# Kernel optimization log

Hardware: AMD Instinct MI355X
Metric: run time of the kernel (lower is better)

Reference implementation:

```python
import jax, jax.numpy as jnp
import numpy as np

N, OBS, H, M, L = 512, 32, 128, 128, 3


def _w(key, shape, fan_in):
    return jax.random.normal(key, shape, dtype=jnp.float32) / np.sqrt(fan_in)


def setup_inputs() -> dict:
    key = jax.random.key(0)
    ks = iter(jax.random.split(key, 64))
    inp = {}
    inp["obs"] = jax.random.normal(next(ks), (N, OBS), dtype=jnp.float32)
    inp["pos"] = jax.random.uniform(next(ks), (N, 2), dtype=jnp.float32)
    # encoder: obs_dim -> H -> H -> H
    inp["enc_W1"] = _w(next(ks), (H, OBS), OBS); inp["enc_b1"] = jnp.zeros((H,), jnp.float32)
    inp["enc_W2"] = _w(next(ks), (H, H), H);     inp["enc_b2"] = jnp.zeros((H,), jnp.float32)
    inp["enc_W3"] = _w(next(ks), (H, H), H);     inp["enc_b3"] = jnp.zeros((H,), jnp.float32)
    # per-layer message MLPs: (2H+1) -> M -> M -> M, stacked over L layers
    inp["msg_W1"] = _w(next(ks), (L, M, 2 * H + 1), 2 * H + 1); inp["msg_b1"] = jnp.zeros((L, M), jnp.float32)
    inp["msg_W2"] = _w(next(ks), (L, M, M), M);                 inp["msg_b2"] = jnp.zeros((L, M), jnp.float32)
    inp["msg_W3"] = _w(next(ks), (L, M, M), M);                 inp["msg_b3"] = jnp.zeros((L, M), jnp.float32)
    # per-layer update MLPs: (H+M) -> H -> H -> H, stacked over L layers
    inp["upd_W1"] = _w(next(ks), (L, H, H + M), H + M); inp["upd_b1"] = jnp.zeros((L, H), jnp.float32)
    inp["upd_W2"] = _w(next(ks), (L, H, H), H);         inp["upd_b2"] = jnp.zeros((L, H), jnp.float32)
    inp["upd_W3"] = _w(next(ks), (L, H, H), H);         inp["upd_b3"] = jnp.zeros((L, H), jnp.float32)
    return inp


def _mlp3(x, W1, b1, W2, b2, W3, b3):
    h = jax.nn.relu(x @ W1.T + b1)
    h = jax.nn.relu(h @ W2.T + b2)
    return h @ W3.T + b3


def reference(obs, pos, enc_W1, enc_b1, enc_W2, enc_b2, enc_W3, enc_b3,
              msg_W1, msg_b1, msg_W2, msg_b2, msg_W3, msg_b3,
              upd_W1, upd_b1, upd_W2, upd_b2, upd_W3, upd_b3):
    n = obs.shape[0]
    h = enc_W1.shape[0]
    z = _mlp3(obs, enc_W1, enc_b1, enc_W2, enc_b2, enc_W3, enc_b3)  # (N, H)
    # pairwise distances; guard diagonal sqrt(0) for grad safety, then zero it
    diff = pos[:, None, :] - pos[None, :, :]                  # (N, N, 2)
    sq = jnp.sum(diff * diff, axis=-1)                        # (N, N)
    eye = jnp.eye(n, dtype=pos.dtype)
    dist = jnp.sqrt(jnp.where(eye > 0, 1.0, sq)) * (1.0 - eye)
    nondiag = (1.0 - eye)[:, :, None]
    n_layers = msg_W1.shape[0]
    for l in range(n_layers):
        W1 = msg_W1[l]
        Wi, Wj, wd = W1[:, :h], W1[:, h:2 * h], W1[:, 2 * h]  # split concat [z_i, z_j, d]
        A = z @ Wi.T                                          # (N, M) receiver term
        B = z @ Wj.T                                          # (N, M) sender term
        h1 = jax.nn.relu(A[:, None, :] + B[None, :, :] + dist[:, :, None] * wd + msg_b1[l])  # (N, N, M)
        h2 = jax.nn.relu(jnp.einsum('ijm,km->ijk', h1, msg_W2[l]) + msg_b2[l])
        m = jnp.einsum('ijm,km->ijk', h2, msg_W3[l]) + msg_b3[l]
        m = m * nondiag                                       # exclude j == i
        msum = jnp.sum(m, axis=1)                             # (N, M) sum over senders j
        z = _mlp3(jnp.concatenate([z, msum], axis=-1),
                  upd_W1[l], upd_b1[l], upd_W2[l], upd_b2[l], upd_W3[l], upd_b3[l])
    return z
```

## Files before the change

### kernel.cpp

```cpp
#include <hip/hip_runtime.h>

#define NA 512
#define NOBS 32
#define NH 128

typedef const float* fp32p;
typedef __attribute__((ext_vector_type(8))) short bf16x8;
typedef __attribute__((ext_vector_type(4))) float f32x4;

__device__ __forceinline__ short f2bf(float f) {
    union { float f; unsigned u; } v; v.f = f;
    unsigned r = v.u + 0x7fffu + ((v.u >> 16) & 1u);
    return (short)(r >> 16);
}

__device__ __forceinline__ bf16x8 wfrag_f4(const float* p) {
    float4 u = *(const float4*)p;
    float4 v = *(const float4*)(p + 4);
    bf16x8 f;
    f[0] = f2bf(u.x); f[1] = f2bf(u.y); f[2] = f2bf(u.z); f[3] = f2bf(u.w);
    f[4] = f2bf(v.x); f[5] = f2bf(v.y); f[6] = f2bf(v.z); f[7] = f2bf(v.w);
    return f;
}

#define HSTR 136

__global__ __launch_bounds__(128) void encoder_kernel(
    fp32p obs, fp32p W1, fp32p b1, fp32p W2, fp32p b2, fp32p W3, fp32p b3,
    float* __restrict__ z) {
    __shared__ float xs[NOBS];
    __shared__ float h1s[NH];
    __shared__ float h2s[NH];
    const int i = blockIdx.x, t = threadIdx.x;
    if (t < NOBS) xs[t] = obs[i * NOBS + t];
    __syncthreads();
    float a = b1[t];
    for (int k = 0; k < NOBS; ++k) a += xs[k] * W1[t * NOBS + k];
    h1s[t] = fmaxf(a, 0.0f);
    __syncthreads();
    a = b2[t];
    for (int k = 0; k < NH; ++k) a += h1s[k] * W2[t * NH + k];
    h2s[t] = fmaxf(a, 0.0f);
    __syncthreads();
    a = b3[t];
    for (int k = 0; k < NH; ++k) a += h2s[k] * W3[t * NH + k];
    z[i * NH + t] = a;
}

__global__ __launch_bounds__(128) void ab_kernel(
    const float* __restrict__ z, fp32p W1l, float* __restrict__ A, float* __restrict__ B) {
    __shared__ float zs[NH];
    const int i = blockIdx.x, m = threadIdx.x;
    zs[m] = z[i * NH + m];
    __syncthreads();
    const float* wr = W1l + m * 257;
    float a = 0.0f, b = 0.0f;
    for (int k = 0; k < NH; ++k) {
        float zk = zs[k];
        a += zk * wr[k];
        b += zk * wr[NH + k];
    }
    A[i * NH + m] = a;
    B[i * NH + m] = b;
}

__global__ __launch_bounds__(512) void msg_upd_kernel(
    const float* __restrict__ A, const float* __restrict__ B,
    fp32p pos, const float* __restrict__ zin,
    fp32p W1l, fp32p b1, fp32p W2, fp32p b2, fp32p W3, fp32p b3,
    fp32p uW1, fp32p ub1, fp32p uW2, fp32p ub2, fp32p uW3, fp32p ub3,
    fp32p msgW1n, int do_ab,
    float* __restrict__ zout, float* __restrict__ An, float* __restrict__ Bn) {
    const int i = blockIdx.x;
    const int t = threadIdx.x;
    const int lane = t & 63;
    const int w = t >> 6;
    const int q = lane >> 4;
    const int c = lane & 15;
    const int ncol = w * 16 + c;

    __shared__ short h1s[64 * HSTR];
    __shared__ short h2s[64 * HSTR];
    __shared__ float distrow[NA];
    __shared__ float amrow[NH];
    __shared__ float wdsr[NH];
    __shared__ float xs2[2 * NH];
    __shared__ float part[4 * NH];
    __shared__ float part2[4 * NH];
    __shared__ float hx[NH], hy[NH], hz[NH];

    if (t < NH) {
        amrow[t] = A[i * NH + t] + b1[t];
        wdsr[t]  = W1l[t * 257 + 256];
        xs2[t] = zin[(size_t)i * NH + t];
    }
    {
        const float2 pi = *(const float2*)&pos[2 * i];
        const float2 pj = *(const float2*)&pos[2 * t];
        const float dx = pi.x - pj.x, dy = pi.y - pj.y;
        const float s = dx * dx + dy * dy;
        distrow[t] = (t == i) ? 0.0f : sqrtf(s);
    }

    bf16x8 w2f[4], w3f[4];
    {
        const float* w2r = W2 + (size_t)ncol * NH + q * 8;
        const float* w3r = W3 + (size_t)ncol * NH + q * 8;
        #pragma unroll
        for (int kb = 0; kb < 4; ++kb) {
            w2f[kb] = wfrag_f4(w2r + kb * 32);
            w3f[kb] = wfrag_f4(w3r + kb * 32);
        }
    }
    const float b2n = b2[ncol];
    const float b3n = b3[ncol];

    const int m2 = lane * 2;
    float psum = 0.0f;

    for (int c8 = 0; c8 < 8; ++c8) {
        const int j0 = c8 * 64;
        __syncthreads();

        {
            const float am0 = amrow[m2],     am1 = amrow[m2 + 1];
            const float wd0 = wdsr[m2],      wd1 = wdsr[m2 + 1];
            #pragma unroll
            for (int rr = 0; rr < 8; ++rr) {
                const int row = rr * 8 + w;
                const int jg  = j0 + row;
                const float2 bv = *(const float2*)&B[(size_t)jg * NH + m2];
                const float d = distrow[jg];
                const float v0 = fmaxf(am0 + bv.x + d * wd0, 0.0f);
                const float v1 = fmaxf(am1 + bv.y + d * wd1, 0.0f);
                const unsigned p = (unsigned)(unsigned short)f2bf(v0) |
                                   ((unsigned)(unsigned short)f2bf(v1) << 16);
                *(unsigned*)&h1s[row * HSTR + m2] = p;
            }
        }
        __syncthreads();

        #pragma unroll
        for (int jt = 0; jt < 4; ++jt) {
            f32x4 acc = {0.f, 0.f, 0.f, 0.f};
            const short* arow = &h1s[(jt * 16 + c) * HSTR + q * 8];
            #pragma unroll
            for (int kb = 0; kb < 4; ++kb) {
                bf16x8 a = *(const bf16x8*)(arow + kb * 32);
                acc = __builtin_amdgcn_mfma_f32_16x16x32_bf16(a, w2f[kb], acc, 0, 0, 0);
            }
            #pragma unroll
            for (int r = 0; r < 4; ++r) {
                const int row = jt * 16 + q * 4 + r;
                h2s[row * HSTR + ncol] = f2bf(fmaxf(acc[r] + b2n, 0.0f));
            }
        }
        __syncthreads();

        #pragma unroll
        for (int jt = 0; jt < 4; ++jt) {
            f32x4 acc = {0.f, 0.f, 0.f, 0.f};
            const short* arow = &h2s[(jt * 16 + c) * HSTR + q * 8];
            #pragma unroll
            for (int kb = 0; kb < 4; ++kb) {
                bf16x8 a = *(const bf16x8*)(arow + kb * 32);
                acc = __builtin_amdgcn_mfma_f32_16x16x32_bf16(a, w3f[kb], acc, 0, 0, 0);
            }
            #pragma unroll
            for (int r = 0; r < 4; ++r) {
                const int jg = j0 + jt * 16 + q * 4 + r;
                if (jg != i) psum += acc[r] + b3n;
            }
        }
    }

    psum += __shfl_xor(psum, 16, 64);
    psum += __shfl_xor(psum, 32, 64);
    if (lane < 16) xs2[NH + ncol] = psum;
    __syncthreads();

    const int nn = t >> 2;
    const int ks = t & 3;
    {
        const float* wr = uW1 + (size_t)nn * 256 + ks * 4;
        float p = 0.f;
        #pragma unroll
        for (int it = 0; it < 16; ++it) {
            const float4 wv = *(const float4*)(wr + it * 16);
            const float4 xv = *(const float4*)&xs2[it * 16 + ks * 4];
            p += wv.x * xv.x + wv.y * xv.y + wv.z * xv.z + wv.w * xv.w;
        }
        part[ks * NH + nn] = p;
    }
    __syncthreads();
    if (t < NH)
        hx[t] = fmaxf(ub1[t] + part[t] + part[NH + t] + part[2 * NH + t] + part[3 * NH + t], 0.f);
    __syncthreads();
    {
        const float* wr = uW2 + (size_t)nn * NH + ks * 4;
        float p = 0.f;
        #pragma unroll
        for (int it = 0; it < 8; ++it) {
            const float4 wv = *(const float4*)(wr + it * 16);
            const float4 xv = *(const float4*)&hx[it * 16 + ks * 4];
            p += wv.x * xv.x + wv.y * xv.y + wv.z * xv.z + wv.w * xv.w;
        }
        part[ks * NH + nn] = p;
    }
    __syncthreads();
    if (t < NH)
        hy[t] = fmaxf(ub2[t] + part[t] + part[NH + t] + part[2 * NH + t] + part[3 * NH + t], 0.f);
    __syncthreads();
    {
        const float* wr = uW3 + (size_t)nn * NH + ks * 4;
        float p = 0.f;
        #pragma unroll
        for (int it = 0; it < 8; ++it) {
            const float4 wv = *(const float4*)(wr + it * 16);
            const float4 xv = *(const float4*)&hy[it * 16 + ks * 4];
            p += wv.x * xv.x + wv.y * xv.y + wv.z * xv.z + wv.w * xv.w;
        }
        part[ks * NH + nn] = p;
    }
    __syncthreads();
    if (t < NH) {
        const float v = ub3[t] + part[t] + part[NH + t] + part[2 * NH + t] + part[3 * NH + t];
        zout[(size_t)i * NH + t] = v;
        hz[t] = v;
    }
    if (!do_ab) return;
    __syncthreads();
    {
        const float* pr = msgW1n + (size_t)nn * 257;
        float pa = 0.f, pb = 0.f;
        #pragma unroll
        for (int it = 0; it < 8; ++it) {
            #pragma unroll
            for (int j = 0; j < 4; ++j) {
                const int k = it * 16 + ks * 4 + j;
                const float x = hz[k];
                pa += x * pr[k];
                pb += x * pr[NH + k];
            }
        }
        part[ks * NH + nn] = pa;
        part2[ks * NH + nn] = pb;
    }
    __syncthreads();
    if (t < NH) {
        An[(size_t)i * NH + t] = part[t] + part[NH + t] + part[2 * NH + t] + part[3 * NH + t];
        Bn[(size_t)i * NH + t] = part2[t] + part2[NH + t] + part2[2 * NH + t] + part2[3 * NH + t];
    }
}

extern "C" void kernel_launch(void* const* d_in, const int* in_sizes, int n_in,
                              void* d_out, int out_size, void* d_ws, size_t ws_size,
                              hipStream_t stream) {
    fp32p obs   = (fp32p)d_in[0];
    fp32p pos   = (fp32p)d_in[1];
    fp32p encW1 = (fp32p)d_in[2];  fp32p encb1 = (fp32p)d_in[3];
    fp32p encW2 = (fp32p)d_in[4];  fp32p encb2 = (fp32p)d_in[5];
    fp32p encW3 = (fp32p)d_in[6];  fp32p encb3 = (fp32p)d_in[7];
    fp32p msgW1 = (fp32p)d_in[8];  fp32p msgb1 = (fp32p)d_in[9];
    fp32p msgW2 = (fp32p)d_in[10]; fp32p msgb2 = (fp32p)d_in[11];
    fp32p msgW3 = (fp32p)d_in[12]; fp32p msgb3 = (fp32p)d_in[13];
    fp32p updW1 = (fp32p)d_in[14]; fp32p updb1 = (fp32p)d_in[15];
    fp32p updW2 = (fp32p)d_in[16]; fp32p updb2 = (fp32p)d_in[17];
    fp32p updW3 = (fp32p)d_in[18]; fp32p updb3 = (fp32p)d_in[19];

    float* ws = (float*)d_ws;
    float* zA = ws;
    float* zB = zA + NA * NH;
    float* A0 = zB + NA * NH;
    float* B0 = A0 + NA * NH;
    float* A1 = B0 + NA * NH;
    float* B1 = A1 + NA * NH;

    encoder_kernel<<<NA, 128, 0, stream>>>(obs, encW1, encb1, encW2, encb2,
                                           encW3, encb3, zA);
    ab_kernel<<<NA, 128, 0, stream>>>(zA, msgW1, A0, B0);

    float* zin = zA;  float* zout = zB;
    float* Ac = A0;   float* Bc = B0;
    float* An = A1;   float* Bn = B1;
    for (int l = 0; l < 3; ++l) {
        const int do_ab = (l < 2);
        float* dst = (l == 2) ? (float*)d_out : zout;
        msg_upd_kernel<<<NA, 512, 0, stream>>>(Ac, Bc, pos, zin,
            msgW1 + (size_t)l * 128 * 257, msgb1 + l * 128,
            msgW2 + (size_t)l * 128 * 128, msgb2 + l * 128,
            msgW3 + (size_t)l * 128 * 128, msgb3 + l * 128,
            updW1 + (size_t)l * 256 * 128, updb1 + l * 128,
            updW2 + (size_t)l * 128 * 128, updb2 + l * 128,
            updW3 + (size_t)l * 128 * 128, updb3 + l * 128,
            msgW1 + (size_t)(l + 1 < 3 ? l + 1 : 0) * 128 * 257, do_ab,
            dst, An, Bn);
        float* tmp;
        tmp = zin; zin = zout; zout = tmp;
        tmp = Ac; Ac = An; An = tmp;
        tmp = Bc; Bc = Bn; Bn = tmp;
    }
}
```

Baseline: 239.5 us.

## Switch message MLP to 32x32 MFMA tiles and fuse encoder with A/B projection

The message MLP GEMMs now use 32x32x16 bf16 MFMA instructions, with each wave computing a 32-row by 32-column tile. Previously each wave ran four 16x16x32 tiles. This cuts the instruction count and the number of LDS A-fragment reads per output, at the cost of more weight-fragment registers and an extra LDS reduction plus barrier across the two row groups. Separately, the encoder and the first A/B projection are merged into one 512-thread kernel that splits each dot product four ways, removing a launch and the global round-trip of z. The dispatch order and total work are otherwise unchanged.

```diff
diff --git a/kernel.cpp b/kernel.cpp
--- a/kernel.cpp
+++ b/kernel.cpp
@@ -6,7 +6,7 @@
 
 typedef const float* fp32p;
 typedef __attribute__((ext_vector_type(8))) short bf16x8;
-typedef __attribute__((ext_vector_type(4))) float f32x4;
+typedef __attribute__((ext_vector_type(16))) float f32x16;
 
 __device__ __forceinline__ short f2bf(float f) {
     union { float f; unsigned u; } v; v.f = f;
@@ -25,43 +25,88 @@
 
 #define HSTR 136
 
-__global__ __launch_bounds__(128) void encoder_kernel(
-    fp32p obs, fp32p W1, fp32p b1, fp32p W2, fp32p b2, fp32p W3, fp32p b3,
-    float* __restrict__ z) {
-    __shared__ float xs[NOBS];
-    __shared__ float h1s[NH];
-    __shared__ float h2s[NH];
-    const int i = blockIdx.x, t = threadIdx.x;
-    if (t < NOBS) xs[t] = obs[i * NOBS + t];
-    __syncthreads();
-    float a = b1[t];
-    for (int k = 0; k < NOBS; ++k) a += xs[k] * W1[t * NOBS + k];
-    h1s[t] = fmaxf(a, 0.0f);
-    __syncthreads();
-    a = b2[t];
-    for (int k = 0; k < NH; ++k) a += h1s[k] * W2[t * NH + k];
-    h2s[t] = fmaxf(a, 0.0f);
-    __syncthreads();
-    a = b3[t];
-    for (int k = 0; k < NH; ++k) a += h2s[k] * W3[t * NH + k];
-    z[i * NH + t] = a;
-}
-
-__global__ __launch_bounds__(128) void ab_kernel(
-    const float* __restrict__ z, fp32p W1l, float* __restrict__ A, float* __restrict__ B) {
-    __shared__ float zs[NH];
-    const int i = blockIdx.x, m = threadIdx.x;
-    zs[m] = z[i * NH + m];
-    __syncthreads();
-    const float* wr = W1l + m * 257;
-    float a = 0.0f, b = 0.0f;
-    for (int k = 0; k < NH; ++k) {
-        float zk = zs[k];
-        a += zk * wr[k];
-        b += zk * wr[NH + k];
-    }
-    A[i * NH + m] = a;
-    B[i * NH + m] = b;
+__global__ __launch_bounds__(512) void enc_ab_kernel(
+    fp32p obs, fp32p eW1, fp32p eb1, fp32p eW2, fp32p eb2, fp32p eW3, fp32p eb3,
+    fp32p mW1, float* __restrict__ z, float* __restrict__ A, float* __restrict__ B) {
+    const int i = blockIdx.x;
+    const int t = threadIdx.x;
+    const int nn = t >> 2;
+    const int ks = t & 3;
+
+    __shared__ float xs0[NOBS];
+    __shared__ float part[4 * NH];
+    __shared__ float part2[4 * NH];
+    __shared__ float hx[NH], hy[NH], zz[NH];
+
+    if (t < NOBS) xs0[t] = obs[(size_t)i * NOBS + t];
+    __syncthreads();
+    {
+        const float* wr = eW1 + (size_t)nn * NOBS + ks * 8;
+        const float4 w0 = *(const float4*)wr;
+        const float4 w1 = *(const float4*)(wr + 4);
+        const float4 x0 = *(const float4*)&xs0[ks * 8];
+        const float4 x1 = *(const float4*)&xs0[ks * 8 + 4];
+        part[ks * NH + nn] = w0.x * x0.x + w0.y * x0.y + w0.z * x0.z + w0.w * x0.w +
+                             w1.x * x1.x + w1.y * x1.y + w1.z * x1.z + w1.w * x1.w;
+    }
+    __syncthreads();
+    if (t < NH)
+        hx[t] = fmaxf(eb1[t] + part[t] + part[NH + t] + part[2 * NH + t] + part[3 * NH + t], 0.f);
+    __syncthreads();
+    {
+        const float* wr = eW2 + (size_t)nn * NH + ks * 4;
+        float p = 0.f;
+        #pragma unroll
+        for (int it = 0; it < 8; ++it) {
+            const float4 wv = *(const float4*)(wr + it * 16);
+            const float4 xv = *(const float4*)&hx[it * 16 + ks * 4];
+            p += wv.x * xv.x + wv.y * xv.y + wv.z * xv.z + wv.w * xv.w;
+        }
+        part[ks * NH + nn] = p;
+    }
+    __syncthreads();
+    if (t < NH)
+        hy[t] = fmaxf(eb2[t] + part[t] + part[NH + t] + part[2 * NH + t] + part[3 * NH + t], 0.f);
+    __syncthreads();
+    {
+        const float* wr = eW3 + (size_t)nn * NH + ks * 4;
+        float p = 0.f;
+        #pragma unroll
+        for (int it = 0; it < 8; ++it) {
+            const float4 wv = *(const float4*)(wr + it * 16);
+            const float4 xv = *(const float4*)&hy[it * 16 + ks * 4];
+            p += wv.x * xv.x + wv.y * xv.y + wv.z * xv.z + wv.w * xv.w;
+        }
+        part[ks * NH + nn] = p;
+    }
+    __syncthreads();
+    if (t < NH) {
+        const float v = eb3[t] + part[t] + part[NH + t] + part[2 * NH + t] + part[3 * NH + t];
+        z[(size_t)i * NH + t] = v;
+        zz[t] = v;
+    }
+    __syncthreads();
+    {
+        const float* pr = mW1 + (size_t)nn * 257;
+        float pa = 0.f, pb = 0.f;
+        #pragma unroll
+        for (int it = 0; it < 8; ++it) {
+            #pragma unroll
+            for (int j = 0; j < 4; ++j) {
+                const int k = it * 16 + ks * 4 + j;
+                const float x = zz[k];
+                pa += x * pr[k];
+                pb += x * pr[NH + k];
+            }
+        }
+        part[ks * NH + nn] = pa;
+        part2[ks * NH + nn] = pb;
+    }
+    __syncthreads();
+    if (t < NH) {
+        A[(size_t)i * NH + t] = part[t] + part[NH + t] + part[2 * NH + t] + part[3 * NH + t];
+        B[(size_t)i * NH + t] = part2[t] + part2[NH + t] + part2[2 * NH + t] + part2[3 * NH + t];
+    }
 }
 
 __global__ __launch_bounds__(512) void msg_upd_kernel(
@@ -75,9 +120,11 @@
     const int t = threadIdx.x;
     const int lane = t & 63;
     const int w = t >> 6;
-    const int q = lane >> 4;
-    const int c = lane & 15;
-    const int ncol = w * 16 + c;
+    const int g   = w >> 2;
+    const int cg  = w & 3;
+    const int l32 = lane & 31;
+    const int lhi = lane >> 5;
+    const int ncol = cg * 32 + l32;
 
     __shared__ short h1s[64 * HSTR];
     __shared__ short h2s[64 * HSTR];
@@ -102,14 +149,14 @@
         distrow[t] = (t == i) ? 0.0f : sqrtf(s);
     }
 
-    bf16x8 w2f[4], w3f[4];
-    {
-        const float* w2r = W2 + (size_t)ncol * NH + q * 8;
-        const float* w3r = W3 + (size_t)ncol * NH + q * 8;
-        #pragma unroll
-        for (int kb = 0; kb < 4; ++kb) {
-            w2f[kb] = wfrag_f4(w2r + kb * 32);
-            w3f[kb] = wfrag_f4(w3r + kb * 32);
+    bf16x8 w2f[8], w3f[8];
+    {
+        const float* w2r = W2 + (size_t)ncol * NH + lhi * 8;
+        const float* w3r = W3 + (size_t)ncol * NH + lhi * 8;
+        #pragma unroll
+        for (int kb = 0; kb < 8; ++kb) {
+            w2f[kb] = wfrag_f4(w2r + kb * 16);
+            w3f[kb] = wfrag_f4(w3r + kb * 16);
         }
     }
     const float b2n = b2[ncol];
@@ -140,43 +187,47 @@
         }
         __syncthreads();
 
-        #pragma unroll
-        for (int jt = 0; jt < 4; ++jt) {
-            f32x4 acc = {0.f, 0.f, 0.f, 0.f};
-            const short* arow = &h1s[(jt * 16 + c) * HSTR + q * 8];
-            #pragma unroll
-            for (int kb = 0; kb < 4; ++kb) {
-                bf16x8 a = *(const bf16x8*)(arow + kb * 32);
-                acc = __builtin_amdgcn_mfma_f32_16x16x32_bf16(a, w2f[kb], acc, 0, 0, 0);
-            }
-            #pragma unroll
-            for (int r = 0; r < 4; ++r) {
-                const int row = jt * 16 + q * 4 + r;
-                h2s[row * HSTR + ncol] = f2bf(fmaxf(acc[r] + b2n, 0.0f));
+        {
+            f32x16 acc;
+            #pragma unroll
+            for (int r = 0; r < 16; ++r) acc[r] = 0.f;
+            const short* arow = &h1s[(g * 32 + l32) * HSTR + lhi * 8];
+            #pragma unroll
+            for (int kb = 0; kb < 8; ++kb) {
+                bf16x8 a = *(const bf16x8*)(arow + kb * 16);
+                acc = __builtin_amdgcn_mfma_f32_32x32x16_bf16(a, w2f[kb], acc, 0, 0, 0);
+            }
+            #pragma unroll
+            for (int r = 0; r < 16; ++r) {
+                const int row = (r & 3) + 8 * (r >> 2) + 4 * lhi;
+                h2s[(g * 32 + row) * HSTR + ncol] = f2bf(fmaxf(acc[r] + b2n, 0.0f));
             }
         }
         __syncthreads();
 
-        #pragma unroll
-        for (int jt = 0; jt < 4; ++jt) {
-            f32x4 acc = {0.f, 0.f, 0.f, 0.f};
-            const short* arow = &h2s[(jt * 16 + c) * HSTR + q * 8];
-            #pragma unroll
-            for (int kb = 0; kb < 4; ++kb) {
-                bf16x8 a = *(const bf16x8*)(arow + kb * 32);
-                acc = __builtin_amdgcn_mfma_f32_16x16x32_bf16(a, w3f[kb], acc, 0, 0, 0);
-            }
-            #pragma unroll
-            for (int r = 0; r < 4; ++r) {
-                const int jg = j0 + jt * 16 + q * 4 + r;
+        {
+            f32x16 acc;
+            #pragma unroll
+            for (int r = 0; r < 16; ++r) acc[r] = 0.f;
+            const short* arow = &h2s[(g * 32 + l32) * HSTR + lhi * 8];
+            #pragma unroll
+            for (int kb = 0; kb < 8; ++kb) {
+                bf16x8 a = *(const bf16x8*)(arow + kb * 16);
+                acc = __builtin_amdgcn_mfma_f32_32x32x16_bf16(a, w3f[kb], acc, 0, 0, 0);
+            }
+            #pragma unroll
+            for (int r = 0; r < 16; ++r) {
+                const int row = (r & 3) + 8 * (r >> 2) + 4 * lhi;
+                const int jg = j0 + g * 32 + row;
                 if (jg != i) psum += acc[r] + b3n;
             }
         }
     }
 
-    psum += __shfl_xor(psum, 16, 64);
     psum += __shfl_xor(psum, 32, 64);
-    if (lane < 16) xs2[NH + ncol] = psum;
+    if (lane < 32) part[g * NH + cg * 32 + lane] = psum;
+    __syncthreads();
+    if (t < NH) xs2[NH + t] = part[t] + part[NH + t];
     __syncthreads();
 
     const int nn = t >> 2;
@@ -276,9 +327,8 @@
     float* A1 = B0 + NA * NH;
     float* B1 = A1 + NA * NH;
 
-    encoder_kernel<<<NA, 128, 0, stream>>>(obs, encW1, encb1, encW2, encb2,
-                                           encW3, encb3, zA);
-    ab_kernel<<<NA, 128, 0, stream>>>(zA, msgW1, A0, B0);
+    enc_ab_kernel<<<NA, 512, 0, stream>>>(obs, encW1, encb1, encW2, encb2,
+                                          encW3, encb3, msgW1, zA, A0, B0);
 
     float* zin = zA;  float* zout = zB;
     float* Ac = A0;   float* Bc = B0;
```

New measurement: 274.0 us. +14.4%, slower.
